# Optimization experiments

Hardware: AMD Instinct MI355X
Metric: run time of the kernel (lower is better)

The kernel has to match this reference:

```python
import jax, jax.numpy as jnp
import numpy as np

B, S, H, NH = 2, 2048, 1024, 16
D = H // NH

def setup_inputs() -> dict:
    key = jax.random.key(0)
    ks = jax.random.split(key, 9)
    s = 1.0 / np.sqrt(H)
    return {
        "x": jax.random.normal(ks[0], (B, S, H), jnp.float32),
        "wq": jax.random.uniform(ks[1], (H, H), jnp.float32, -s, s),
        "bq": jax.random.uniform(ks[2], (H,), jnp.float32, -s, s),
        "wk": jax.random.uniform(ks[3], (H, H), jnp.float32, -s, s),
        "bk": jax.random.uniform(ks[4], (H,), jnp.float32, -s, s),
        "wv": jax.random.uniform(ks[5], (H, H), jnp.float32, -s, s),
        "bv": jax.random.uniform(ks[6], (H,), jnp.float32, -s, s),
        "wo": jax.random.uniform(ks[7], (H, H), jnp.float32, -s, s),
        "bo": jax.random.uniform(ks[8], (H,), jnp.float32, -s, s),
    }

def _split_heads(t):
    # [B, S, H] -> [B, NH, S, D]
    return t.reshape(B, S, NH, D).transpose(0, 2, 1, 3)

def reference(x, wq, bq, wk, bk, wv, bv, wo, bo):
    q = _split_heads(x @ wq.T + bq)
    k = _split_heads(x @ wk.T + bk)
    v = _split_heads(x @ wv.T + bv)
    scores = jnp.einsum('bhqd,bhkd->bhqk', q, k) / jnp.sqrt(jnp.float32(D))
    attn = jax.nn.softmax(scores, axis=-1)  # full [B,NH,S,S] materialized as in source
    ctx = jnp.einsum('bhqk,bhkd->bhqd', attn, v)
    concat = ctx.transpose(0, 2, 1, 3).reshape(B, S, H)
    return concat @ wo.T + bo
```

## Files before the change

kernel.cpp:

```cpp
#include <hip/hip_runtime.h>
#include <cstdint>

typedef unsigned short u16;
typedef __attribute__((ext_vector_type(8))) short short8;
typedef __attribute__((ext_vector_type(8))) _Float16 half8;
typedef __attribute__((ext_vector_type(2))) __fp16 fp16x2;
typedef __attribute__((ext_vector_type(4))) float f32x4;
typedef __attribute__((ext_vector_type(4))) unsigned short ushort4v;

#if __has_builtin(__builtin_amdgcn_exp2f)
#define EXP2F(x) __builtin_amdgcn_exp2f(x)
#else
#define EXP2F(x) exp2f(x)
#endif

#define SYNC_DRAIN() do { \
  asm volatile("s_waitcnt vmcnt(0) lgkmcnt(0)" ::: "memory"); \
  __syncthreads(); \
} while (0)

__device__ inline u16 f2h(float f) {
  union { _Float16 h; u16 u; } v;
  v.h = (_Float16)f;
  return v.u;
}

__device__ inline void gl2lds16(const void* g, void* l) {
  __builtin_amdgcn_global_load_lds(
      (const __attribute__((address_space(1))) unsigned int*)(unsigned long long)(uintptr_t)g,
      (__attribute__((address_space(3))) unsigned int*)(unsigned int)(uintptr_t)l,
      16, 0, 0);
}


__global__ __launch_bounds__(256) void cvt_kernel(
    const float* __restrict__ x,
    const float* __restrict__ wq, const float* __restrict__ wk,
    const float* __restrict__ wv, const float* __restrict__ wo,
    u16* __restrict__ xb, u16* __restrict__ wqb, u16* __restrict__ wkb,
    u16* __restrict__ wvb, u16* __restrict__ wob) {
  const int y = blockIdx.y;
  const int Q = 1 << 20;
  const float* src;
  u16* dst;
  if (y < 4)       { src = x + y * Q; dst = xb + y * Q; }
  else if (y == 4) { src = wq; dst = wqb; }
  else if (y == 5) { src = wk; dst = wkb; }
  else if (y == 6) { src = wv; dst = wvb; }
  else             { src = wo; dst = wob; }
  const int i = (blockIdx.x * 256 + threadIdx.x) * 8;
  float4 a = *(const float4*)(src + i);
  float4 b = *(const float4*)(src + i + 4);
  short8 o;
  o[0] = (short)f2h(a.x); o[1] = (short)f2h(a.y);
  o[2] = (short)f2h(a.z); o[3] = (short)f2h(a.w);
  o[4] = (short)f2h(b.x); o[5] = (short)f2h(b.y);
  o[6] = (short)f2h(b.z); o[7] = (short)f2h(b.w);
  const int j = (i & ~63) | (((((i >> 3) & 7) ^ ((i >> 10) & 7))) << 3);
  *(short8*)(dst + j) = o;
}

__global__ __launch_bounds__(256, 2) void gemm_qkv(
    const u16* __restrict__ xb,
    const u16* __restrict__ wqb, const u16* __restrict__ wkb, const u16* __restrict__ wvb,
    const float* __restrict__ bq, const float* __restrict__ bk, const float* __restrict__ bv,
    u16* __restrict__ qo, u16* __restrict__ ko, u16* __restrict__ vto) {
  __shared__ u16 smem[40960];
  u16* As = smem;
  u16* Bs = smem + 16384;
  const int tid = threadIdx.x, lane = tid & 63;
  const int wid = tid >> 6;
  const int l15 = lane & 15, lg = lane >> 4;
  const int m0 = blockIdx.y * 128, n0 = blockIdx.x * 64;
  const int sw = ((l15 & 7) << 3);
  const u16* Wz[3] = {wqb, wkb, wvb};

  f32x4 acc[3][2][4] = {};

#pragma unroll
  for (int i = 0; i < 4; ++i) {
    int c = i * 256 + tid;
    gl2lds16(xb + (m0 + (c >> 3)) * 1024 + (c & 7) * 8, As + c * 8);
  }
#pragma unroll
  for (int z = 0; z < 3; ++z)
#pragma unroll
    for (int i = 0; i < 2; ++i) {
      int c = i * 256 + tid;
      gl2lds16(Wz[z] + (n0 + (c >> 3)) * 1024 + (c & 7) * 8, Bs + z * 4096 + c * 8);
    }

  for (int k0 = 0; k0 < 1024; k0 += 64) {
    const int p = (k0 >> 6) & 1;
    SYNC_DRAIN();
    if (k0 < 960) {
      u16* An = As + (1 - p) * 8192;
      u16* Bn = Bs + (1 - p) * 12288;
#pragma unroll
      for (int i = 0; i < 4; ++i) {
        int c = i * 256 + tid;
        gl2lds16(xb + (m0 + (c >> 3)) * 1024 + k0 + 64 + (c & 7) * 8, An + c * 8);
      }
#pragma unroll
      for (int z = 0; z < 3; ++z)
#pragma unroll
        for (int i = 0; i < 2; ++i) {
          int c = i * 256 + tid;
          gl2lds16(Wz[z] + (n0 + (c >> 3)) * 1024 + k0 + 64 + (c & 7) * 8, Bn + z * 4096 + c * 8);
        }
    }
    const u16* Ap = As + p * 8192;
    const u16* Bp = Bs + p * 12288;
#pragma unroll
    for (int kk = 0; kk < 2; ++kk) {
      half8 af[2], bf[3][4];
#pragma unroll
      for (int mb = 0; mb < 2; ++mb)
        af[mb] = *(const half8*)(Ap + (wid * 32 + mb * 16 + l15) * 64 + ((((kk * 4 + lg) << 3)) ^ sw));
#pragma unroll
      for (int z = 0; z < 3; ++z)
#pragma unroll
        for (int nb = 0; nb < 4; ++nb)
          bf[z][nb] = *(const half8*)(Bp + z * 4096 + (nb * 16 + l15) * 64 + ((((kk * 4 + lg) << 3)) ^ sw));
#pragma unroll
      for (int z = 0; z < 3; ++z)
#pragma unroll
        for (int mb = 0; mb < 2; ++mb)
#pragma unroll
          for (int nb = 0; nb < 4; ++nb)
            acc[z][mb][nb] = __builtin_amdgcn_mfma_f32_16x16x32_f16(af[mb], bf[z][nb], acc[z][mb][nb], 0, 0, 0);
    }
  }

  const float cexp = 0.18033688011112042f;

#pragma unroll
  for (int mb = 0; mb < 2; ++mb)
#pragma unroll
    for (int nb = 0; nb < 4; ++nb)
#pragma unroll
      for (int r = 0; r < 4; ++r) {
        int m = m0 + wid * 32 + mb * 16 + lg * 4 + r;
        int n = n0 + nb * 16 + l15;
        float v = (acc[0][mb][nb][r] + bq[n]) * cexp;
        int b = m >> 11, s = m & 2047, hh = n >> 6, d = n & 63;
        qo[((b * 16 + hh) * 2048 + s) * 64 + d] = f2h(v);
      }

#pragma unroll
  for (int mb = 0; mb < 2; ++mb)
#pragma unroll
    for (int nb = 0; nb < 4; ++nb)
#pragma unroll
      for (int r = 0; r < 4; ++r) {
        int m = m0 + wid * 32 + mb * 16 + lg * 4 + r;
        int n = n0 + nb * 16 + l15;
        float v = acc[1][mb][nb][r] + bk[n];
        int b = m >> 11, s = m & 2047, hh = n >> 6, d = n & 63;
        int dcol = (((d >> 3) ^ (s & 7)) << 3) | (d & 7);
        ko[((b * 16 + hh) * 2048 + s) * 64 + dcol] = f2h(v);
      }

  SYNC_DRAIN();
  {
    u16* wbuf = smem + (wid >> 1) * 4608;
#pragma unroll
    for (int mb = 0; mb < 2; ++mb)
#pragma unroll
      for (int nb = 0; nb < 4; ++nb) {
        int n = n0 + nb * 16 + l15;
        float bn = bv[n];
        int dl = nb * 16 + l15;
#pragma unroll
        for (int r = 0; r < 4; ++r) {
          int sig = (wid & 1) * 32 + lg * 8 + mb * 4 + r;
          wbuf[dl * 72 + sig] = f2h(acc[2][mb][nb][r] + bn);
        }
      }
    SYNC_DRAIN();
    int hh = n0 >> 6;
    int bb = m0 >> 11;
    int sbase = m0 & 2047;
#pragma unroll
    for (int i = 0; i < 4; ++i) {
      int idx = i * 256 + tid;
      int p2 = idx >> 9, rem = idx & 511;
      int dl = rem >> 3, c = rem & 7;
      short8 vv = *(const short8*)(smem + p2 * 4608 + dl * 72 + c * 8);
      int cs = c ^ (dl & 7);
      *(short8*)(vto + ((bb * 16 + hh) * 64 + dl) * 2048 + sbase + p2 * 64 + cs * 8) = vv;
    }
  }
}

__global__ __launch_bounds__(256, 2) void attn_kernel(
    const u16* __restrict__ qg, const u16* __restrict__ kg,
    const u16* __restrict__ vtg, u16* __restrict__ ctxg) {
  const int h = blockIdx.x, qt = blockIdx.y, b = blockIdx.z;
  const int bh = b * 16 + h;
  const u16* Qg = qg + (bh * 2048 + qt * 128) * 64;
  const u16* Kg = kg + bh * 2048 * 64;
  const u16* Vg = vtg + bh * 64 * 2048;

  __shared__ u16 SP[128 * 72];
  __shared__ u16 KV[2][8192];

  const int tid = threadIdx.x, lane = tid & 63, wid = tid >> 6;
  const int l15 = lane & 15, lg = lane >> 4;
  const int row0 = wid * 32;
  const int sw = ((l15 & 7) << 3);

  half8 qf[2][2];
#pragma unroll
  for (int qtile = 0; qtile < 2; ++qtile)
#pragma unroll
    for (int kk = 0; kk < 2; ++kk)
      qf[qtile][kk] = *(const half8*)(Qg + (row0 + qtile * 16 + l15) * 64 + kk * 32 + lg * 8);

  half8 ones8;
#pragma unroll
  for (int j = 0; j < 8; ++j) ones8[j] = (_Float16)1.0f;

#pragma unroll
  for (int i = 0; i < 2; ++i) {
    int c = i * 256 + tid;
    gl2lds16(Kg + c * 8, &KV[0][c * 8]);
    gl2lds16(Vg + (c >> 3) * 2048 + (c & 7) * 8, &KV[0][4096 + c * 8]);
  }

  f32x4 acc[4][2] = {};
  f32x4 accl[2] = {};

  for (int kt = 0; kt < 32; ++kt) {
    const int p = kt & 1;
    SYNC_DRAIN();
    if (kt < 31) {
#pragma unroll
      for (int i = 0; i < 2; ++i) {
        int c = i * 256 + tid;
        gl2lds16(Kg + (kt + 1) * 4096 + c * 8, &KV[1 - p][c * 8]);
        gl2lds16(Vg + (c >> 3) * 2048 + (kt + 1) * 64 + (c & 7) * 8, &KV[1 - p][4096 + c * 8]);
      }
    }
    const u16* Ks = &KV[p][0];
    const u16* Vts = &KV[p][4096];

    f32x4 sc[4][2] = {};
#pragma unroll
    for (int kk = 0; kk < 2; ++kk) {
      half8 kf[4];
#pragma unroll
      for (int ktile = 0; ktile < 4; ++ktile)
        kf[ktile] = *(const half8*)(Ks + (ktile * 16 + l15) * 64 + ((((kk * 4 + lg) << 3)) ^ sw));
#pragma unroll
      for (int ktile = 0; ktile < 4; ++ktile)
#pragma unroll
        for (int qtile = 0; qtile < 2; ++qtile)
          sc[ktile][qtile] = __builtin_amdgcn_mfma_f32_16x16x32_f16(kf[ktile], qf[qtile][kk], sc[ktile][qtile], 0, 0, 0);
    }

    half8 pf[2][2];
#pragma unroll
    for (int sl = 0; sl < 2; ++sl)
#pragma unroll
      for (int qtile = 0; qtile < 2; ++qtile) {
        union { half8 h; fp16x2 h2[4]; } pu;
        float a0 = EXP2F(sc[sl * 2][qtile][0]),     a1 = EXP2F(sc[sl * 2][qtile][1]);
        float a2 = EXP2F(sc[sl * 2][qtile][2]),     a3 = EXP2F(sc[sl * 2][qtile][3]);
        float b0 = EXP2F(sc[sl * 2 + 1][qtile][0]), b1 = EXP2F(sc[sl * 2 + 1][qtile][1]);
        float b2 = EXP2F(sc[sl * 2 + 1][qtile][2]), b3 = EXP2F(sc[sl * 2 + 1][qtile][3]);
        pu.h2[0] = __builtin_amdgcn_cvt_pkrtz(a0, a1);
        pu.h2[1] = __builtin_amdgcn_cvt_pkrtz(a2, a3);
        pu.h2[2] = __builtin_amdgcn_cvt_pkrtz(b0, b1);
        pu.h2[3] = __builtin_amdgcn_cvt_pkrtz(b2, b3);
        pf[sl][qtile] = pu.h;
      }

#pragma unroll
    for (int sl = 0; sl < 2; ++sl) {
      half8 vf[4];
#pragma unroll
      for (int dtile = 0; dtile < 4; ++dtile)
        vf[dtile] = *(const half8*)(Vts + (dtile * 16 + l15) * 64 + ((((sl * 4 + lg) << 3)) ^ sw));
#pragma unroll
      for (int dtile = 0; dtile < 4; ++dtile)
#pragma unroll
        for (int qtile = 0; qtile < 2; ++qtile)
          acc[dtile][qtile] = __builtin_amdgcn_mfma_f32_16x16x32_f16(vf[dtile], pf[sl][qtile], acc[dtile][qtile], 0, 0, 0);
#pragma unroll
      for (int qtile = 0; qtile < 2; ++qtile)
        accl[qtile] = __builtin_amdgcn_mfma_f32_16x16x32_f16(ones8, pf[sl][qtile], accl[qtile], 0, 0, 0);
    }
  }

#pragma unroll
  for (int qtile = 0; qtile < 2; ++qtile) {
    float inv = 1.0f / accl[qtile][0];
#pragma unroll
    for (int dtile = 0; dtile < 4; ++dtile) {
      ushort4v pk;
#pragma unroll
      for (int r = 0; r < 4; ++r)
        pk[r] = f2h(acc[dtile][qtile][r] * inv);
      *(ushort4v*)(SP + (row0 + qtile * 16 + l15) * 72 + dtile * 16 + lg * 4) = pk;
    }
  }
  SYNC_DRAIN();
#pragma unroll
  for (int i = 0; i < 4; ++i) {
    int idx = i * 64 + lane;
    int rl = idx >> 3, c = idx & 7;
    short8 vv = *(const short8*)(SP + (row0 + rl) * 72 + c * 8);
    int s = qt * 128 + row0 + rl;
    int cs = c ^ (s & 7);
    *(short8*)(ctxg + ((long)b * 2048 + s) * 1024 + h * 64 + cs * 8) = vv;
  }
}

__global__ __launch_bounds__(256) void gemm_out(
    const u16* __restrict__ cb, const u16* __restrict__ wob,
    const float* __restrict__ bo, float* __restrict__ out) {
  __shared__ u16 smem[16384];
  u16* As = smem;
  u16* Bs = smem + 8192;
  const int tid = threadIdx.x, lane = tid & 63;
  const int wid = tid >> 6;
  const int l15 = lane & 15, lg = lane >> 4;
  const int m0 = blockIdx.y * 64, n0 = blockIdx.x * 64;
  const int sw = ((l15 & 7) << 3);

  f32x4 acc[4] = {};

#pragma unroll
  for (int i = 0; i < 2; ++i) {
    int c = i * 256 + tid;
    gl2lds16(cb  + (m0 + (c >> 3)) * 1024 + (c & 7) * 8, As + c * 8);
    gl2lds16(wob + (n0 + (c >> 3)) * 1024 + (c & 7) * 8, Bs + c * 8);
  }

  for (int k0 = 0; k0 < 1024; k0 += 64) {
    const int p = (k0 >> 6) & 1;
    SYNC_DRAIN();
    if (k0 < 960) {
      u16* An = As + (1 - p) * 4096;
      u16* Bn = Bs + (1 - p) * 4096;
#pragma unroll
      for (int i = 0; i < 2; ++i) {
        int c = i * 256 + tid;
        gl2lds16(cb  + (m0 + (c >> 3)) * 1024 + k0 + 64 + (c & 7) * 8, An + c * 8);
        gl2lds16(wob + (n0 + (c >> 3)) * 1024 + k0 + 64 + (c & 7) * 8, Bn + c * 8);
      }
    }
    const u16* Ap = As + p * 4096;
    const u16* Bp = Bs + p * 4096;
#pragma unroll
    for (int kk = 0; kk < 2; ++kk) {
      half8 af, bf[4];
      af = *(const half8*)(Ap + (wid * 16 + l15) * 64 + ((((kk * 4 + lg) << 3)) ^ sw));
#pragma unroll
      for (int nb = 0; nb < 4; ++nb)
        bf[nb] = *(const half8*)(Bp + (nb * 16 + l15) * 64 + ((((kk * 4 + lg) << 3)) ^ sw));
#pragma unroll
      for (int nb = 0; nb < 4; ++nb)
        acc[nb] = __builtin_amdgcn_mfma_f32_16x16x32_f16(af, bf[nb], acc[nb], 0, 0, 0);
    }
  }

#pragma unroll
  for (int nb = 0; nb < 4; ++nb)
#pragma unroll
    for (int r = 0; r < 4; ++r) {
      int m = m0 + wid * 16 + lg * 4 + r;
      int n = n0 + nb * 16 + l15;
      out[m * 1024 + n] = acc[nb][r] + bo[n];
    }
}

extern "C" void kernel_launch(void* const* d_in, const int* in_sizes, int n_in,
                              void* d_out, int out_size, void* d_ws, size_t ws_size,
                              hipStream_t stream) {
  const float* x  = (const float*)d_in[0];
  const float* wq = (const float*)d_in[1];
  const float* bq = (const float*)d_in[2];
  const float* wk = (const float*)d_in[3];
  const float* bk = (const float*)d_in[4];
  const float* wv = (const float*)d_in[5];
  const float* bv = (const float*)d_in[6];
  const float* wo = (const float*)d_in[7];
  const float* bo = (const float*)d_in[8];

  if (ws_size < (size_t)24 * 1024 * 1024 * 2) return;
  u16* xb   = (u16*)d_ws;
  u16* wqb  = xb  + (4u << 20);
  u16* wkb  = wqb + (1u << 20);
  u16* wvb  = wkb + (1u << 20);
  u16* wob  = wvb + (1u << 20);
  u16* qb   = wob + (1u << 20);
  u16* kb   = qb  + (4u << 20);
  u16* vtb  = kb  + (4u << 20);
  u16* ctxb = vtb + (4u << 20);

  cvt_kernel<<<dim3(512, 8, 1), 256, 0, stream>>>(x, wq, wk, wv, wo, xb, wqb, wkb, wvb, wob);
  gemm_qkv<<<dim3(16, 32, 1), 256, 0, stream>>>(xb, wqb, wkb, wvb, bq, bk, bv, qb, kb, vtb);
  attn_kernel<<<dim3(16, 16, 2), 256, 0, stream>>>(qb, kb, vtb, ctxb);
  gemm_out<<<dim3(16, 64, 1), 256, 0, stream>>>(ctxb, wob, bo, (float*)d_out);
}
```

Measured before the change: 170.8 us.

## Split attention KV range across two blocks and combine partials in a new kernel

```diff
diff --git a/kernel.cpp b/kernel.cpp
--- a/kernel.cpp
+++ b/kernel.cpp
@@ -23,6 +23,12 @@
   union { _Float16 h; u16 u; } v;
   v.h = (_Float16)f;
   return v.u;
+}
+
+__device__ inline float h2f(u16 u) {
+  union { u16 u; _Float16 h; } v;
+  v.u = u;
+  return (float)v.h;
 }
 
 __device__ inline void gl2lds16(const void* g, void* l) {
@@ -195,14 +201,15 @@
 
 __global__ __launch_bounds__(256, 2) void attn_kernel(
     const u16* __restrict__ qg, const u16* __restrict__ kg,
-    const u16* __restrict__ vtg, u16* __restrict__ ctxg) {
-  const int h = blockIdx.x, qt = blockIdx.y, b = blockIdx.z;
+    const u16* __restrict__ vtg, u16* __restrict__ po, float* __restrict__ pl) {
+  const int h = blockIdx.x, qt = blockIdx.y;
+  const int b = blockIdx.z >> 1, half = blockIdx.z & 1;
   const int bh = b * 16 + h;
+  const int kbase = half * 16;
   const u16* Qg = qg + (bh * 2048 + qt * 128) * 64;
   const u16* Kg = kg + bh * 2048 * 64;
   const u16* Vg = vtg + bh * 64 * 2048;
 
-  __shared__ u16 SP[128 * 72];
   __shared__ u16 KV[2][8192];
 
   const int tid = threadIdx.x, lane = tid & 63, wid = tid >> 6;
@@ -224,22 +231,23 @@
 #pragma unroll
   for (int i = 0; i < 2; ++i) {
     int c = i * 256 + tid;
-    gl2lds16(Kg + c * 8, &KV[0][c * 8]);
-    gl2lds16(Vg + (c >> 3) * 2048 + (c & 7) * 8, &KV[0][4096 + c * 8]);
+    gl2lds16(Kg + kbase * 4096 + c * 8, &KV[0][c * 8]);
+    gl2lds16(Vg + (c >> 3) * 2048 + kbase * 64 + (c & 7) * 8, &KV[0][4096 + c * 8]);
   }
 
   f32x4 acc[4][2] = {};
   f32x4 accl[2] = {};
 
-  for (int kt = 0; kt < 32; ++kt) {
-    const int p = kt & 1;
+  for (int it = 0; it < 16; ++it) {
+    const int p = it & 1;
     SYNC_DRAIN();
-    if (kt < 31) {
+    if (it < 15) {
+      const int ktn = kbase + it + 1;
 #pragma unroll
       for (int i = 0; i < 2; ++i) {
         int c = i * 256 + tid;
-        gl2lds16(Kg + (kt + 1) * 4096 + c * 8, &KV[1 - p][c * 8]);
-        gl2lds16(Vg + (c >> 3) * 2048 + (kt + 1) * 64 + (c & 7) * 8, &KV[1 - p][4096 + c * 8]);
+        gl2lds16(Kg + ktn * 4096 + c * 8, &KV[1 - p][c * 8]);
+        gl2lds16(Vg + (c >> 3) * 2048 + ktn * 64 + (c & 7) * 8, &KV[1 - p][4096 + c * 8]);
       }
     }
     const u16* Ks = &KV[p][0];
@@ -295,25 +303,56 @@
 
 #pragma unroll
   for (int qtile = 0; qtile < 2; ++qtile) {
-    float inv = 1.0f / accl[qtile][0];
+    int sg = qt * 128 + row0 + qtile * 16 + l15;
 #pragma unroll
     for (int dtile = 0; dtile < 4; ++dtile) {
       ushort4v pk;
 #pragma unroll
       for (int r = 0; r < 4; ++r)
-        pk[r] = f2h(acc[dtile][qtile][r] * inv);
-      *(ushort4v*)(SP + (row0 + qtile * 16 + l15) * 72 + dtile * 16 + lg * 4) = pk;
-    }
-  }
+        pk[r] = f2h(acc[dtile][qtile][r]);
+      long idx = ((long)((half * 32 + bh) * 16 + dtile * 4 + lg)) * 8192 + sg * 4;
+      *(ushort4v*)(po + idx) = pk;
+    }
+    if (lane < 16)
+      pl[half * 65536 + bh * 2048 + qt * 128 + row0 + qtile * 16 + lane] = accl[qtile][0];
+  }
+}
+
+__global__ __launch_bounds__(256) void combine_kernel(
+    const u16* __restrict__ po, const float* __restrict__ pl,
+    u16* __restrict__ ctxg) {
+  __shared__ u16 L[2][8192];
+  const int bh = blockIdx.x, s0 = blockIdx.y * 128;
+  const int tid = threadIdx.x;
+  const int b = bh >> 4, h = bh & 15;
+
+#pragma unroll
+  for (int hf = 0; hf < 2; ++hf)
+#pragma unroll
+    for (int i = 0; i < 4; ++i) {
+      int c = i * 256 + tid;
+      gl2lds16(po + ((long)((hf * 32 + bh) * 16 + (c >> 6))) * 8192 + s0 * 4 + (c & 63) * 8,
+               &L[hf][c * 8]);
+    }
   SYNC_DRAIN();
-#pragma unroll
-  for (int i = 0; i < 4; ++i) {
-    int idx = i * 64 + lane;
-    int rl = idx >> 3, c = idx & 7;
-    short8 vv = *(const short8*)(SP + (row0 + rl) * 72 + c * 8);
-    int s = qt * 128 + row0 + rl;
-    int cs = c ^ (s & 7);
-    *(short8*)(ctxg + ((long)b * 2048 + s) * 1024 + h * 64 + cs * 8) = vv;
+
+  const int sl = tid >> 1, dbase = (tid & 1) * 32;
+  const int sg = s0 + sl;
+  float inv = 1.0f / (pl[bh * 2048 + sg] + pl[65536 + bh * 2048 + sg]);
+  const int soff = (sl >> 1) * 8 + (sl & 1) * 4;
+#pragma unroll
+  for (int j = 0; j < 4; ++j) {
+    int d0 = dbase + j * 8;
+    short8 o;
+#pragma unroll
+    for (int e = 0; e < 8; ++e) {
+      int d = d0 + e;
+      int li = (d >> 2) * 512 + soff + (d & 3);
+      o[e] = (short)f2h((h2f(L[0][li]) + h2f(L[1][li])) * inv);
+    }
+    int c = d0 >> 3;
+    int cs = c ^ (sg & 7);
+    *(short8*)(ctxg + ((long)b * 2048 + sg) * 1024 + h * 64 + cs * 8) = o;
   }
 }
 
@@ -389,7 +428,7 @@
   const float* wo = (const float*)d_in[7];
   const float* bo = (const float*)d_in[8];
 
-  if (ws_size < (size_t)24 * 1024 * 1024 * 2) return;
+  if (ws_size < (size_t)66 * 1024 * 1024) return;
   u16* xb   = (u16*)d_ws;
   u16* wqb  = xb  + (4u << 20);
   u16* wkb  = wqb + (1u << 20);
@@ -399,9 +438,12 @@
   u16* kb   = qb  + (4u << 20);
   u16* vtb  = kb  + (4u << 20);
   u16* ctxb = vtb + (4u << 20);
+  u16* po   = ctxb + (4u << 20);
+  float* pl = (float*)(po + (8u << 20));
 
   cvt_kernel<<<dim3(512, 8, 1), 256, 0, stream>>>(x, wq, wk, wv, wo, xb, wqb, wkb, wvb, wob);
   gemm_qkv<<<dim3(16, 32, 1), 256, 0, stream>>>(xb, wqb, wkb, wvb, bq, bk, bv, qb, kb, vtb);
-  attn_kernel<<<dim3(16, 16, 2), 256, 0, stream>>>(qb, kb, vtb, ctxb);
+  attn_kernel<<<dim3(16, 16, 4), 256, 0, stream>>>(qb, kb, vtb, po, pl);
+  combine_kernel<<<dim3(32, 16, 1), 256, 0, stream>>>(po, pl, ctxb);
   gemm_out<<<dim3(16, 64, 1), 256, 0, stream>>>(ctxb, wob, bo, (float*)d_out);
 }
```

Result: slower. 176.4 us (+3.3%).

## Process 256 query rows per attention block to reuse K/V tiles

Applied to the files above, without the earlier changes.

```diff
diff --git a/kernel.cpp b/kernel.cpp
--- a/kernel.cpp
+++ b/kernel.cpp
@@ -193,29 +193,31 @@
   }
 }
 
-__global__ __launch_bounds__(256, 2) void attn_kernel(
+__global__ __launch_bounds__(256, 1) void attn_kernel(
     const u16* __restrict__ qg, const u16* __restrict__ kg,
     const u16* __restrict__ vtg, u16* __restrict__ ctxg) {
   const int h = blockIdx.x, qt = blockIdx.y, b = blockIdx.z;
   const int bh = b * 16 + h;
-  const u16* Qg = qg + (bh * 2048 + qt * 128) * 64;
+  const u16* Qg = qg + (bh * 2048 + qt * 256) * 64;
   const u16* Kg = kg + bh * 2048 * 64;
   const u16* Vg = vtg + bh * 64 * 2048;
 
-  __shared__ u16 SP[128 * 72];
   __shared__ u16 KV[2][8192];
+  u16* SP = &KV[0][0];
 
   const int tid = threadIdx.x, lane = tid & 63, wid = tid >> 6;
   const int l15 = lane & 15, lg = lane >> 4;
   const int row0 = wid * 32;
   const int sw = ((l15 & 7) << 3);
 
-  half8 qf[2][2];
-#pragma unroll
-  for (int qtile = 0; qtile < 2; ++qtile)
-#pragma unroll
-    for (int kk = 0; kk < 2; ++kk)
-      qf[qtile][kk] = *(const half8*)(Qg + (row0 + qtile * 16 + l15) * 64 + kk * 32 + lg * 8);
+  half8 qf[2][2][2];
+#pragma unroll
+  for (int g = 0; g < 2; ++g)
+#pragma unroll
+    for (int qtile = 0; qtile < 2; ++qtile)
+#pragma unroll
+      for (int kk = 0; kk < 2; ++kk)
+        qf[g][qtile][kk] = *(const half8*)(Qg + (g * 128 + row0 + qtile * 16 + l15) * 64 + kk * 32 + lg * 8);
 
   half8 ones8;
 #pragma unroll
@@ -228,8 +230,8 @@
     gl2lds16(Vg + (c >> 3) * 2048 + (c & 7) * 8, &KV[0][4096 + c * 8]);
   }
 
-  f32x4 acc[4][2] = {};
-  f32x4 accl[2] = {};
+  f32x4 acc[2][4][2] = {};
+  f32x4 accl[2][2] = {};
 
   for (int kt = 0; kt < 32; ++kt) {
     const int p = kt & 1;
@@ -245,75 +247,83 @@
     const u16* Ks = &KV[p][0];
     const u16* Vts = &KV[p][4096];
 
-    f32x4 sc[4][2] = {};
-#pragma unroll
-    for (int kk = 0; kk < 2; ++kk) {
-      half8 kf[4];
-#pragma unroll
-      for (int ktile = 0; ktile < 4; ++ktile)
-        kf[ktile] = *(const half8*)(Ks + (ktile * 16 + l15) * 64 + ((((kk * 4 + lg) << 3)) ^ sw));
-#pragma unroll
-      for (int ktile = 0; ktile < 4; ++ktile)
+#pragma unroll
+    for (int g = 0; g < 2; ++g) {
+      f32x4 sc[4][2] = {};
+#pragma unroll
+      for (int kk = 0; kk < 2; ++kk) {
+        half8 kf[4];
+#pragma unroll
+        for (int ktile = 0; ktile < 4; ++ktile)
+          kf[ktile] = *(const half8*)(Ks + (ktile * 16 + l15) * 64 + ((((kk * 4 + lg) << 3)) ^ sw));
+#pragma unroll
+        for (int ktile = 0; ktile < 4; ++ktile)
+#pragma unroll
+          for (int qtile = 0; qtile < 2; ++qtile)
+            sc[ktile][qtile] = __builtin_amdgcn_mfma_f32_16x16x32_f16(kf[ktile], qf[g][qtile][kk], sc[ktile][qtile], 0, 0, 0);
+      }
+
+      half8 pf[2][2];
+#pragma unroll
+      for (int sl = 0; sl < 2; ++sl)
+#pragma unroll
+        for (int qtile = 0; qtile < 2; ++qtile) {
+          union { half8 h; fp16x2 h2[4]; } pu;
+          float a0 = EXP2F(sc[sl * 2][qtile][0]),     a1 = EXP2F(sc[sl * 2][qtile][1]);
+          float a2 = EXP2F(sc[sl * 2][qtile][2]),     a3 = EXP2F(sc[sl * 2][qtile][3]);
+          float b0 = EXP2F(sc[sl * 2 + 1][qtile][0]), b1 = EXP2F(sc[sl * 2 + 1][qtile][1]);
+          float b2 = EXP2F(sc[sl * 2 + 1][qtile][2]), b3 = EXP2F(sc[sl * 2 + 1][qtile][3]);
+          pu.h2[0] = __builtin_amdgcn_cvt_pkrtz(a0, a1);
+          pu.h2[1] = __builtin_amdgcn_cvt_pkrtz(a2, a3);
+          pu.h2[2] = __builtin_amdgcn_cvt_pkrtz(b0, b1);
+          pu.h2[3] = __builtin_amdgcn_cvt_pkrtz(b2, b3);
+          pf[sl][qtile] = pu.h;
+        }
+
+#pragma unroll
+      for (int sl = 0; sl < 2; ++sl) {
+        half8 vf[4];
+#pragma unroll
+        for (int dtile = 0; dtile < 4; ++dtile)
+          vf[dtile] = *(const half8*)(Vts + (dtile * 16 + l15) * 64 + ((((sl * 4 + lg) << 3)) ^ sw));
+#pragma unroll
+        for (int dtile = 0; dtile < 4; ++dtile)
+#pragma unroll
+          for (int qtile = 0; qtile < 2; ++qtile)
+            acc[g][dtile][qtile] = __builtin_amdgcn_mfma_f32_16x16x32_f16(vf[dtile], pf[sl][qtile], acc[g][dtile][qtile], 0, 0, 0);
 #pragma unroll
         for (int qtile = 0; qtile < 2; ++qtile)
-          sc[ktile][qtile] = __builtin_amdgcn_mfma_f32_16x16x32_f16(kf[ktile], qf[qtile][kk], sc[ktile][qtile], 0, 0, 0);
-    }
-
-    half8 pf[2][2];
-#pragma unroll
-    for (int sl = 0; sl < 2; ++sl)
-#pragma unroll
-      for (int qtile = 0; qtile < 2; ++qtile) {
-        union { half8 h; fp16x2 h2[4]; } pu;
-        float a0 = EXP2F(sc[sl * 2][qtile][0]),     a1 = EXP2F(sc[sl * 2][qtile][1]);
-        float a2 = EXP2F(sc[sl * 2][qtile][2]),     a3 = EXP2F(sc[sl * 2][qtile][3]);
-        float b0 = EXP2F(sc[sl * 2 + 1][qtile][0]), b1 = EXP2F(sc[sl * 2 + 1][qtile][1]);
-        float b2 = EXP2F(sc[sl * 2 + 1][qtile][2]), b3 = EXP2F(sc[sl * 2 + 1][qtile][3]);
-        pu.h2[0] = __builtin_amdgcn_cvt_pkrtz(a0, a1);
-        pu.h2[1] = __builtin_amdgcn_cvt_pkrtz(a2, a3);
-        pu.h2[2] = __builtin_amdgcn_cvt_pkrtz(b0, b1);
-        pu.h2[3] = __builtin_amdgcn_cvt_pkrtz(b2, b3);
-        pf[sl][qtile] = pu.h;
-      }
-
-#pragma unroll
-    for (int sl = 0; sl < 2; ++sl) {
-      half8 vf[4];
-#pragma unroll
-      for (int dtile = 0; dtile < 4; ++dtile)
-        vf[dtile] = *(const half8*)(Vts + (dtile * 16 + l15) * 64 + ((((sl * 4 + lg) << 3)) ^ sw));
-#pragma unroll
-      for (int dtile = 0; dtile < 4; ++dtile)
-#pragma unroll
-        for (int qtile = 0; qtile < 2; ++qtile)
-          acc[dtile][qtile] = __builtin_amdgcn_mfma_f32_16x16x32_f16(vf[dtile], pf[sl][qtile], acc[dtile][qtile], 0, 0, 0);
-#pragma unroll
-      for (int qtile = 0; qtile < 2; ++qtile)
-        accl[qtile] = __builtin_amdgcn_mfma_f32_16x16x32_f16(ones8, pf[sl][qtile], accl[qtile], 0, 0, 0);
-    }
-  }
-
-#pragma unroll
-  for (int qtile = 0; qtile < 2; ++qtile) {
-    float inv = 1.0f / accl[qtile][0];
-#pragma unroll
-    for (int dtile = 0; dtile < 4; ++dtile) {
-      ushort4v pk;
-#pragma unroll
-      for (int r = 0; r < 4; ++r)
-        pk[r] = f2h(acc[dtile][qtile][r] * inv);
-      *(ushort4v*)(SP + (row0 + qtile * 16 + l15) * 72 + dtile * 16 + lg * 4) = pk;
-    }
-  }
+          accl[g][qtile] = __builtin_amdgcn_mfma_f32_16x16x32_f16(ones8, pf[sl][qtile], accl[g][qtile], 0, 0, 0);
+      }
+    }
+  }
+
   SYNC_DRAIN();
 #pragma unroll
-  for (int i = 0; i < 4; ++i) {
-    int idx = i * 64 + lane;
-    int rl = idx >> 3, c = idx & 7;
-    short8 vv = *(const short8*)(SP + (row0 + rl) * 72 + c * 8);
-    int s = qt * 128 + row0 + rl;
-    int cs = c ^ (s & 7);
-    *(short8*)(ctxg + ((long)b * 2048 + s) * 1024 + h * 64 + cs * 8) = vv;
+  for (int g = 0; g < 2; ++g) {
+    if (g) SYNC_DRAIN();
+#pragma unroll
+    for (int qtile = 0; qtile < 2; ++qtile) {
+      float inv = 1.0f / accl[g][qtile][0];
+#pragma unroll
+      for (int dtile = 0; dtile < 4; ++dtile) {
+        ushort4v pk;
+#pragma unroll
+        for (int r = 0; r < 4; ++r)
+          pk[r] = f2h(acc[g][dtile][qtile][r] * inv);
+        *(ushort4v*)(SP + (row0 + qtile * 16 + l15) * 72 + dtile * 16 + lg * 4) = pk;
+      }
+    }
+    SYNC_DRAIN();
+#pragma unroll
+    for (int i = 0; i < 4; ++i) {
+      int idx = i * 64 + lane;
+      int rl = idx >> 3, c = idx & 7;
+      short8 vv = *(const short8*)(SP + (row0 + rl) * 72 + c * 8);
+      int s = qt * 256 + g * 128 + row0 + rl;
+      int cs = c ^ (s & 7);
+      *(short8*)(ctxg + ((long)b * 2048 + s) * 1024 + h * 64 + cs * 8) = vv;
+    }
   }
 }
 
@@ -402,6 +412,6 @@
 
   cvt_kernel<<<dim3(512, 8, 1), 256, 0, stream>>>(x, wq, wk, wv, wo, xb, wqb, wkb, wvb, wob);
   gemm_qkv<<<dim3(16, 32, 1), 256, 0, stream>>>(xb, wqb, wkb, wvb, bq, bk, bv, qb, kb, vtb);
-  attn_kernel<<<dim3(16, 16, 2), 256, 0, stream>>>(qb, kb, vtb, ctxb);
+  attn_kernel<<<dim3(16, 8, 2), 256, 0, stream>>>(qb, kb, vtb, ctxb);
   gemm_out<<<dim3(16, 64, 1), 256, 0, stream>>>(ctxb, wob, bo, (float*)d_out);
 }
```

Result: slower. 174.8 us (+2.3%).
